# Kernel optimization log

Hardware: AMD Instinct MI355X
Metric: run time of the kernel (lower is better)

The kernel has to match this reference:

```python
import jax, jax.numpy as jnp
import numpy as np

TAU = 2.0  # LIF membrane time constant (spikingjelly default)
SCALE = 0.125

@jax.custom_vjp
def heaviside(x):
    return (x >= 0).astype(x.dtype)

def _hv_fwd(x):
    return heaviside(x), x

def _hv_bwd(x, g):
    s = jax.nn.sigmoid(4.0 * x)  # sigmoid surrogate, alpha=4
    return (g * 4.0 * s * (1.0 - s),)

heaviside.defvjp(_hv_fwd, _hv_bwd)

def lif(x, v_th):
    """Multi-step LIF over leading time axis. x: [T, ...]. decay_input, hard reset to 0."""
    def step(v, xt):
        v = v + (xt - v) / TAU
        s = heaviside(v - v_th)
        return v * (1.0 - s), s
    return jax.lax.scan(step, jnp.zeros_like(x[0]), x)[1]

def conv1x1(x, w, b=None):
    # x: [T,B,C,N], w: [O,C]
    y = jnp.einsum('oc,tbcn->tbon', w, x)
    if b is not None:
        y = y + b[None, None, :, None]
    return y

def bn(x, p, eps=1e-5):
    # inference-mode BatchNorm1d over channel axis; p: [4,C] = gamma,beta,mean,var
    g, b, m, v = p[0], p[1], p[2], p[3]
    inv = g / jnp.sqrt(v + eps)
    return x * inv[None, None, :, None] + (b - m * inv)[None, None, :, None]

def setup_inputs() -> dict:
    key = jax.random.key(0)
    ks = jax.random.split(key, 10)
    T, B, C, H, W = 4, 32, 512, 16, 16
    wscale = 1.0 / np.sqrt(C)
    def bn_params(k):
        k1, k2, k3, k4 = jax.random.split(k, 4)
        gamma = 1.0 + 0.1 * jax.random.normal(k1, (C,))
        beta = 0.1 * jax.random.normal(k2, (C,))
        mean = 0.1 * jax.random.normal(k3, (C,))
        var = 1.0 + 0.1 * jax.random.uniform(k4, (C,))
        return jnp.stack([gamma, beta, mean, var])
    return {
        'x': jax.random.normal(ks[0], (T, B, C, H, W), dtype=jnp.float32),
        'res_attn': jnp.zeros((1,), dtype=jnp.float32),
        'q_w': wscale * jax.random.normal(ks[1], (C, C), dtype=jnp.float32),
        'k_w': wscale * jax.random.normal(ks[2], (C, C), dtype=jnp.float32),
        'v_w': wscale * jax.random.normal(ks[3], (C, C), dtype=jnp.float32),
        'proj_w': wscale * jax.random.normal(ks[4], (C, C), dtype=jnp.float32),
        'proj_b': 0.01 * jax.random.normal(ks[5], (C,), dtype=jnp.float32),
        'q_bn': bn_params(ks[6]),
        'k_bn': bn_params(ks[7]),
        'v_bn': bn_params(ks[8]),
        'p_bn': bn_params(ks[9]),
    }

def reference(x, res_attn, q_w, k_w, v_w, proj_w, proj_b, q_bn, k_bn, v_bn, p_bn):
    T, B, C, H, W = x.shape
    num_heads = 8
    d = C // num_heads
    N = H * W
    xf = x.reshape(T, B, C, N)

    def branch(w, p, v_th):
        return lif(bn(conv1x1(xf, w), p), v_th)

    def to_heads(t):  # [T,B,C,N] -> [T,B,h,N,d]
        return t.transpose(0, 1, 3, 2).reshape(T, B, N, num_heads, d).transpose(0, 1, 3, 2, 4)

    q = to_heads(branch(q_w, q_bn, 1.0))
    k = to_heads(branch(k_w, k_bn, 1.0))
    v = to_heads(branch(v_w, v_bn, 1.0))

    # linear (non-softmax) attention: q @ (k^T @ v) * scale
    kv = jnp.einsum('tbhnd,tbhne->tbhde', k, v)
    a = jnp.einsum('tbhnd,tbhde->tbhne', q, kv) * SCALE  # [T,B,h,N,d]

    # [T,B,h,N,d] -> transpose(3,4) -> [T,B,h,d,N] -> [T,B,C,N]
    a = jnp.swapaxes(a, 3, 4).reshape(T, B, C, N)
    a = lif(a, 0.5)  # attn_lif with v_threshold=0.5

    out = conv1x1(a, proj_w, proj_b)
    out = bn(out, p_bn).reshape(T, B, C, H, W)
    out = lif(out, 1.0)
    return out, v
```

## Files before the change

### kernel.cpp

```cpp
#include <hip/hip_runtime.h>
#include <stdint.h>

#define T_ 4
#define B_ 32
#define C_ 512
#define N_ 256
#define NH_ 8
#define NB_ (N_ / 8)
#define BITS_BYTES_ ((size_t)(T_ * B_ * C_) * NB_)

typedef float f32x2 __attribute__((ext_vector_type(2)));

__device__ __forceinline__ f32x2 pk_mul_d(f32x2 a, f32x2 b) {
  f32x2 r;
  asm("v_pk_mul_f32 %0, %1, %2" : "=v"(r) : "v"(a), "v"(b));
  return r;
}
__device__ __forceinline__ f32x2 pk_mul_x(f32x2 a, f32x2 b) {
  f32x2 r;
  asm("v_pk_mul_f32 %0, %1, %2 op_sel:[0,1] op_sel_hi:[1,0]"
      : "=v"(r) : "v"(a), "v"(b));
  return r;
}
__device__ __forceinline__ void pk_add_acc(f32x2& acc, f32x2 p) {
  asm("v_pk_add_f32 %0, %0, %1" : "+v"(acc) : "v"(p));
}
__device__ __forceinline__ void pk_fma_d(f32x2& acc, f32x2 a, f32x2 b) {
  asm("v_pk_fma_f32 %0, %1, %2, %0" : "+v"(acc) : "v"(a), "v"(b));
}
__device__ __forceinline__ void pk_fma_x(f32x2& acc, f32x2 a, f32x2 b) {
  asm("v_pk_fma_f32 %0, %1, %2, %0 op_sel:[0,1,0] op_sel_hi:[1,0,1]"
      : "+v"(acc) : "v"(a), "v"(b));
}


__global__ __launch_bounds__(256, 2) void qkv_gemm_lif(
    const float* __restrict__ x, const float* __restrict__ wq,
    const float* __restrict__ wk, const float* __restrict__ wv,
    const float* __restrict__ bnq, const float* __restrict__ bnk,
    const float* __restrict__ bnv,
    uint8_t* __restrict__ sbits, float* __restrict__ out1) {
#pragma clang fp contract(off)
  const int br = blockIdx.z;
  const int b  = blockIdx.y;
  const int ot = blockIdx.x >> 1, nt = blockIdx.x & 1;
  const float* w = (br == 0) ? wq : (br == 1) ? wk : wv;
  const float* bn = (br == 0) ? bnq : (br == 1) ? bnk : bnv;
  uint8_t* sb = sbits + (size_t)br * BITS_BYTES_;

  const int tid = threadIdx.x;
  const int tx = tid & 15, ty = tid >> 4;
  const int o0 = ot * 64, n0 = nt * 128;

  __shared__ float As[16][64];
  __shared__ float Bs[16][128];

  float inv[4], add[4];
#pragma unroll
  for (int i = 0; i < 4; ++i) {
    int o = o0 + ty * 4 + i;
    float g = bn[o], be = bn[C_ + o], mm = bn[2 * C_ + o], va = bn[3 * C_ + o];
    float iv = g / sqrtf(va + 1e-5f);
    inv[i] = iv;
    add[i] = be - mm * iv;
  }

  float vst[4][8];
#pragma unroll
  for (int i = 0; i < 4; ++i)
#pragma unroll
    for (int j = 0; j < 8; ++j) vst[i][j] = 0.f;

  for (int t = 0; t < T_; ++t) {
    const float* xb = x + (size_t)(t * B_ + b) * (C_ * N_);
    f32x2 acc_d[2][4], acc_x[2][4];
#pragma unroll
    for (int ip = 0; ip < 2; ++ip)
#pragma unroll
      for (int jp = 0; jp < 4; ++jp) {
        acc_d[ip][jp] = (f32x2){0.f, 0.f};
        acc_x[ip][jp] = (f32x2){0.f, 0.f};
      }

    for (int kc = 0; kc < C_; kc += 16) {
      int o = tid & 63, kq = (tid >> 6) * 4;
      float4 a4 = *(const float4*)(w + (size_t)(o0 + o) * C_ + kc + kq);
      int fr = tid >> 5, fq = (tid & 31) * 4;
      int fr2 = (tid + 256) >> 5, fq2 = ((tid + 256) & 31) * 4;
      float4 b40 = *(const float4*)(xb + (size_t)(kc + fr) * N_ + n0 + fq);
      float4 b41 = *(const float4*)(xb + (size_t)(kc + fr2) * N_ + n0 + fq2);
      __syncthreads();
      As[kq + 0][o] = a4.x; As[kq + 1][o] = a4.y;
      As[kq + 2][o] = a4.z; As[kq + 3][o] = a4.w;
      *(float4*)(&Bs[fr][fq]) = b40;
      *(float4*)(&Bs[fr2][fq2]) = b41;
      __syncthreads();
#pragma unroll
      for (int k = 0; k < 16; ++k) {
        float4 av4 = *(const float4*)(&As[k][ty * 4]);
        float4 bq0 = *(const float4*)(&Bs[k][tx * 4]);
        float4 bq1 = *(const float4*)(&Bs[k][64 + tx * 4]);
        f32x2 a2[2] = {(f32x2){av4.x, av4.y}, (f32x2){av4.z, av4.w}};
        f32x2 b2[4] = {(f32x2){bq0.x, bq0.y}, (f32x2){bq0.z, bq0.w},
                       (f32x2){bq1.x, bq1.y}, (f32x2){bq1.z, bq1.w}};
#pragma unroll
        for (int ip = 0; ip < 2; ++ip)
#pragma unroll
          for (int jp = 0; jp < 4; ++jp) {
            f32x2 pd = pk_mul_d(a2[ip], b2[jp]);
            f32x2 px = pk_mul_x(a2[ip], b2[jp]);
            pk_add_acc(acc_d[ip][jp], pd);
            pk_add_acc(acc_x[ip][jp], px);
          }
      }
    }
    __syncthreads();

    {
      size_t tb = (size_t)(t * B_ + b);
      unsigned nibsA = 0, nibsB = 0;
#pragma unroll
      for (int i = 0; i < 4; ++i) {
#pragma unroll
        for (int jj = 0; jj < 8; ++jj) {
          int ip = i >> 1, il = i & 1, jp = jj >> 1, jl = jj & 1;
          float a = (il == jl) ? acc_d[ip][jp][il] : acc_x[ip][jp][il];
          float y0 = a * inv[i];
          float y = y0 + add[i];
          float d = y - vst[i][jj];
          float vs = vst[i][jj] + d * 0.5f;
          unsigned sp = (vs >= 1.0f) ? 1u : 0u;
          vst[i][jj] = sp ? 0.f : vs;
          if (jj < 4) nibsA |= sp << (4 * i + jj);
          else        nibsB |= sp << (4 * i + jj - 4);
        }
      }
      unsigned oA = __shfl_xor(nibsA, 1);
      unsigned oB = __shfl_xor(nibsB, 1);
      int m = tx >> 1;
      if ((tx & 1) == 0) {
#pragma unroll
        for (int i = 0; i < 4; ++i) {
          int o = o0 + ty * 4 + i;
          unsigned byte_ = ((nibsA >> (4 * i)) & 0xF) | (((oA >> (4 * i)) & 0xF) << 4);
          sb[(tb * C_ + o) * NB_ + (n0 >> 3) + m] = (uint8_t)byte_;
        }
      } else {
#pragma unroll
        for (int i = 0; i < 4; ++i) {
          int o = o0 + ty * 4 + i;
          unsigned byte_ = ((oB >> (4 * i)) & 0xF) | (((nibsB >> (4 * i)) & 0xF) << 4);
          sb[(tb * C_ + o) * NB_ + (n0 >> 3) + 8 + m] = (uint8_t)byte_;
        }
      }
      if (br == 2) {
#pragma unroll
        for (int i = 0; i < 4; ++i) {
          int o = o0 + ty * 4 + i;
          int h = o >> 6, dd = o & 63;
          size_t base = ((tb * NH_ + h) * (size_t)N_) * 64 + dd;
#pragma unroll
          for (int jj = 0; jj < 8; ++jj) {
            int n = n0 + ((jj < 4) ? (tx * 4 + jj) : (64 + tx * 4 + jj - 4));
            unsigned sp = (jj < 4) ? ((nibsA >> (4 * i + jj)) & 1u)
                                   : ((nibsB >> (4 * i + jj - 4)) & 1u);
            out1[base + (size_t)n * 64] = sp ? 1.0f : 0.0f;
          }
        }
      }
    }
  }
}

__global__ __launch_bounds__(512, 1) void attn_lif(
    const uint8_t* __restrict__ bits, uint8_t* __restrict__ abits) {
#pragma clang fp contract(off)
  const unsigned long long* qb = (const unsigned long long*)bits;
  const unsigned long long* kb = qb + BITS_BYTES_ / 8;
  const unsigned long long* vb = kb + BITS_BYTES_ / 8;
  unsigned long long* ap = (unsigned long long*)abits;

  const int h = blockIdx.x, b = blockIdx.y;
  const int tid = threadIdx.x;
  const int lane = tid & 63, wave = tid >> 6;
  const int nw = wave & 3, eh = wave >> 2;

  __shared__ unsigned long long kbl[64][4];
  __shared__ unsigned long long vbl[64][4];
  __shared__ float kvl[64][64];

  float state[32];
#pragma unroll
  for (int e = 0; e < 32; ++e) state[e] = 0.f;

  for (int t = 0; t < T_; ++t) {
    size_t row0 = (size_t)(t * B_ + b) * C_ + h * 64;
    {
      int i = tid & 255, c = i >> 2, w = i & 3;
      if (tid < 256) kbl[c][w] = kb[(row0 + c) * 4 + w];
      else           vbl[c][w] = vb[(row0 + c) * 4 + w];
    }
    __syncthreads();
    {
      int d = tid & 63, eb = (tid >> 6) * 8;
#pragma unroll
      for (int e2 = 0; e2 < 8; ++e2) {
        int e = eb + e2;
        int s = 0;
#pragma unroll
        for (int w = 0; w < 4; ++w) s += __popcll(kbl[d][w] & vbl[e][w]);
        kvl[d][e] = (float)s;
      }
    }
    __syncthreads();
    float acc[32];
#pragma unroll
    for (int e = 0; e < 32; ++e) acc[e] = 0.f;
    for (int d = 0; d < 64; ++d) {
      unsigned long long qw = qb[(row0 + d) * 4 + nw];
      float qf = (float)(unsigned)((qw >> lane) & 1ULL);
      const float* kr = &kvl[d][eh * 32];
#pragma unroll
      for (int e = 0; e < 32; ++e) acc[e] = acc[e] + qf * kr[e];
    }
    {
#pragma unroll
      for (int e2 = 0; e2 < 32; ++e2) {
        int e = eh * 32 + e2;
        float a = acc[e2] * 0.125f;
        float d0 = a - state[e2];
        float vs = state[e2] + d0 * 0.5f;
        int sp = (vs >= 0.5f) ? 1 : 0;
        state[e2] = sp ? 0.f : vs;
        unsigned long long m = __ballot(sp);
        if (lane == 0) ap[(row0 + e) * 4 + nw] = m;
      }
    }
    __syncthreads();
  }
}

__global__ __launch_bounds__(256, 2) void proj_gemm_lif(
    const uint8_t* __restrict__ ab, const float* __restrict__ wp,
    const float* __restrict__ pb, const float* __restrict__ bnp,
    float* __restrict__ out0) {
  const int b = blockIdx.y;
  const int ot = blockIdx.x >> 1, nt = blockIdx.x & 1;
  const int tid = threadIdx.x;
  const int tx = tid & 15, ty = tid >> 4;
  const int o0 = ot * 64, n0 = nt * 128;

  __shared__ float As[16][64];
  __shared__ float Bs[16][128];

  float inv[4], add[4], bias[4];
  {
#pragma clang fp contract(off)
#pragma unroll
    for (int i = 0; i < 4; ++i) {
      int o = o0 + ty * 4 + i;
      float g = bnp[o], be = bnp[C_ + o], mm = bnp[2 * C_ + o], va = bnp[3 * C_ + o];
      float iv = g / sqrtf(va + 1e-5f);
      inv[i] = iv;
      add[i] = be - mm * iv;
      bias[i] = pb[o];
    }
  }

  float vst[4][8];
#pragma unroll
  for (int i = 0; i < 4; ++i)
#pragma unroll
    for (int j = 0; j < 8; ++j) vst[i][j] = 0.f;

  for (int t = 0; t < T_; ++t) {
    f32x2 acc_d[2][4], acc_x[2][4];
#pragma unroll
    for (int ip = 0; ip < 2; ++ip)
#pragma unroll
      for (int jp = 0; jp < 4; ++jp) {
        acc_d[ip][jp] = (f32x2){0.f, 0.f};
        acc_x[ip][jp] = (f32x2){0.f, 0.f};
      }
    size_t tb = (size_t)(t * B_ + b);

    for (int kc = 0; kc < C_; kc += 16) {
      {
        int o = tid & 63, kq = (tid >> 6) * 4;
        float4 a4 = *(const float4*)(wp + (size_t)(o0 + o) * C_ + kc + kq);
        As[kq + 0][o] = a4.x; As[kq + 1][o] = a4.y;
        As[kq + 2][o] = a4.z; As[kq + 3][o] = a4.w;
      }
      {
        int r = tid >> 4, q16 = tid & 15;
        uint8_t by = ab[(tb * C_ + kc + r) * NB_ + (n0 >> 3) + q16];
        int nb = q16 * 8;
#pragma unroll
        for (int j = 0; j < 8; ++j) Bs[r][nb + j] = (float)((by >> j) & 1);
      }
      __syncthreads();
#pragma unroll
      for (int k = 0; k < 16; ++k) {
        float4 av4 = *(const float4*)(&As[k][ty * 4]);
        float4 bq0 = *(const float4*)(&Bs[k][tx * 4]);
        float4 bq1 = *(const float4*)(&Bs[k][64 + tx * 4]);
        f32x2 a2[2] = {(f32x2){av4.x, av4.y}, (f32x2){av4.z, av4.w}};
        f32x2 b2[4] = {(f32x2){bq0.x, bq0.y}, (f32x2){bq0.z, bq0.w},
                       (f32x2){bq1.x, bq1.y}, (f32x2){bq1.z, bq1.w}};
#pragma unroll
        for (int ip = 0; ip < 2; ++ip)
#pragma unroll
          for (int jp = 0; jp < 4; ++jp) {
            pk_fma_d(acc_d[ip][jp], a2[ip], b2[jp]);
            pk_fma_x(acc_x[ip][jp], a2[ip], b2[jp]);
          }
      }
      __syncthreads();
    }

    {
#pragma clang fp contract(off)
#pragma unroll
      for (int i = 0; i < 4; ++i) {
        int o = o0 + ty * 4 + i;
        float4 r0, r1;
#pragma unroll
        for (int jj = 0; jj < 8; ++jj) {
          int ip = i >> 1, il = i & 1, jp = jj >> 1, jl = jj & 1;
          float a = (il == jl) ? acc_d[ip][jp][il] : acc_x[ip][jp][il];
          float y1 = a + bias[i];
          float y2 = y1 * inv[i];
          float y = y2 + add[i];
          float d0 = y - vst[i][jj];
          float vs = vst[i][jj] + d0 * 0.5f;
          int sp = (vs >= 1.0f) ? 1 : 0;
          vst[i][jj] = sp ? 0.f : vs;
          if (jj < 4) (&r0.x)[jj] = sp ? 1.0f : 0.0f;
          else        (&r1.x)[jj - 4] = sp ? 1.0f : 0.0f;
        }
        float* dst = out0 + (tb * C_ + o) * N_ + n0;
        *(float4*)(dst + tx * 4) = r0;
        *(float4*)(dst + 64 + tx * 4) = r1;
      }
    }
  }
}


extern "C" void kernel_launch(void* const* d_in, const int* in_sizes, int n_in,
                              void* d_out, int out_size, void* d_ws, size_t ws_size,
                              hipStream_t stream) {
  const float* x   = (const float*)d_in[0];
  const float* qw  = (const float*)d_in[2];
  const float* kw  = (const float*)d_in[3];
  const float* vw  = (const float*)d_in[4];
  const float* pw  = (const float*)d_in[5];
  const float* pbb = (const float*)d_in[6];
  const float* qbn = (const float*)d_in[7];
  const float* kbn = (const float*)d_in[8];
  const float* vbn = (const float*)d_in[9];
  const float* pbn = (const float*)d_in[10];

  uint8_t* bits  = (uint8_t*)d_ws;
  uint8_t* abits = bits + 3 * BITS_BYTES_;

  float* out0 = (float*)d_out;
  float* out1 = out0 + (size_t)T_ * B_ * C_ * N_;

  qkv_gemm_lif<<<dim3(16, 32, 3), dim3(256), 0, stream>>>(
      x, qw, kw, vw, qbn, kbn, vbn, bits, out1);
  attn_lif<<<dim3(8, 32), dim3(512), 0, stream>>>(bits, abits);
  proj_gemm_lif<<<dim3(16, 32), dim3(256), 0, stream>>>(abits, pw, pbb, pbn,
                                                        out0);
}
```

Before: 1.304 ms.

## Double-buffer shared-memory tiles in QKV and projection GEMM kernels

Both GEMM+LIF kernels now use two shared-memory buffers for the A and B tiles. The loads for the next K-chunk are issued from global memory before computing on the current chunk, then stored into the other buffer. This removes one barrier per iteration and hides global load latency behind the FMA loop. In exchange it doubles LDS use per block and adds register pressure from the prefetched values, which may hurt occupancy.

```diff
diff --git a/kernel.cpp b/kernel.cpp
--- a/kernel.cpp
+++ b/kernel.cpp
@@ -52,8 +52,8 @@
   const int tx = tid & 15, ty = tid >> 4;
   const int o0 = ot * 64, n0 = nt * 128;
 
-  __shared__ float As[16][64];
-  __shared__ float Bs[16][128];
+  __shared__ float As[2][16][64];
+  __shared__ float Bs[2][16][128];
 
   float inv[4], add[4];
 #pragma unroll
@@ -71,6 +71,10 @@
 #pragma unroll
     for (int j = 0; j < 8; ++j) vst[i][j] = 0.f;
 
+  const int sa_o = tid & 63, sa_kq = (tid >> 6) * 4;
+  const int fr = tid >> 5, fq = (tid & 31) * 4;
+  const int fr2 = (tid + 256) >> 5, fq2 = ((tid + 256) & 31) * 4;
+
   for (int t = 0; t < T_; ++t) {
     const float* xb = x + (size_t)(t * B_ + b) * (C_ * N_);
     f32x2 acc_d[2][4], acc_x[2][4];
@@ -82,24 +86,32 @@
         acc_x[ip][jp] = (f32x2){0.f, 0.f};
       }
 
-    for (int kc = 0; kc < C_; kc += 16) {
-      int o = tid & 63, kq = (tid >> 6) * 4;
-      float4 a4 = *(const float4*)(w + (size_t)(o0 + o) * C_ + kc + kq);
-      int fr = tid >> 5, fq = (tid & 31) * 4;
-      int fr2 = (tid + 256) >> 5, fq2 = ((tid + 256) & 31) * 4;
-      float4 b40 = *(const float4*)(xb + (size_t)(kc + fr) * N_ + n0 + fq);
-      float4 b41 = *(const float4*)(xb + (size_t)(kc + fr2) * N_ + n0 + fq2);
+    {
+      float4 a4 = *(const float4*)(w + (size_t)(o0 + sa_o) * C_ + 0 + sa_kq);
+      float4 b40 = *(const float4*)(xb + (size_t)(0 + fr) * N_ + n0 + fq);
+      float4 b41 = *(const float4*)(xb + (size_t)(0 + fr2) * N_ + n0 + fq2);
       __syncthreads();
-      As[kq + 0][o] = a4.x; As[kq + 1][o] = a4.y;
-      As[kq + 2][o] = a4.z; As[kq + 3][o] = a4.w;
-      *(float4*)(&Bs[fr][fq]) = b40;
-      *(float4*)(&Bs[fr2][fq2]) = b41;
+      As[0][sa_kq + 0][sa_o] = a4.x; As[0][sa_kq + 1][sa_o] = a4.y;
+      As[0][sa_kq + 2][sa_o] = a4.z; As[0][sa_kq + 3][sa_o] = a4.w;
+      *(float4*)(&Bs[0][fr][fq]) = b40;
+      *(float4*)(&Bs[0][fr2][fq2]) = b41;
       __syncthreads();
+    }
+
+    for (int it = 0; it < 32; ++it) {
+      const int cur = it & 1;
+      float4 a4, b40, b41;
+      if (it < 31) {
+        int kc = (it + 1) * 16;
+        a4  = *(const float4*)(w + (size_t)(o0 + sa_o) * C_ + kc + sa_kq);
+        b40 = *(const float4*)(xb + (size_t)(kc + fr) * N_ + n0 + fq);
+        b41 = *(const float4*)(xb + (size_t)(kc + fr2) * N_ + n0 + fq2);
+      }
 #pragma unroll
       for (int k = 0; k < 16; ++k) {
-        float4 av4 = *(const float4*)(&As[k][ty * 4]);
-        float4 bq0 = *(const float4*)(&Bs[k][tx * 4]);
-        float4 bq1 = *(const float4*)(&Bs[k][64 + tx * 4]);
+        float4 av4 = *(const float4*)(&As[cur][k][ty * 4]);
+        float4 bq0 = *(const float4*)(&Bs[cur][k][tx * 4]);
+        float4 bq1 = *(const float4*)(&Bs[cur][k][64 + tx * 4]);
         f32x2 a2[2] = {(f32x2){av4.x, av4.y}, (f32x2){av4.z, av4.w}};
         f32x2 b2[4] = {(f32x2){bq0.x, bq0.y}, (f32x2){bq0.z, bq0.w},
                        (f32x2){bq1.x, bq1.y}, (f32x2){bq1.z, bq1.w}};
@@ -113,8 +125,15 @@
             pk_add_acc(acc_x[ip][jp], px);
           }
       }
-    }
-    __syncthreads();
+      if (it < 31) {
+        const int nxt = cur ^ 1;
+        As[nxt][sa_kq + 0][sa_o] = a4.x; As[nxt][sa_kq + 1][sa_o] = a4.y;
+        As[nxt][sa_kq + 2][sa_o] = a4.z; As[nxt][sa_kq + 3][sa_o] = a4.w;
+        *(float4*)(&Bs[nxt][fr][fq]) = b40;
+        *(float4*)(&Bs[nxt][fr2][fq2]) = b41;
+        __syncthreads();
+      }
+    }
 
     {
       size_t tb = (size_t)(t * B_ + b);
@@ -250,8 +269,8 @@
   const int tx = tid & 15, ty = tid >> 4;
   const int o0 = ot * 64, n0 = nt * 128;
 
-  __shared__ float As[16][64];
-  __shared__ float Bs[16][128];
+  __shared__ float As[2][16][64];
+  __shared__ float Bs[2][16][128];
 
   float inv[4], add[4], bias[4];
   {
@@ -273,6 +292,9 @@
 #pragma unroll
     for (int j = 0; j < 8; ++j) vst[i][j] = 0.f;
 
+  const int sa_o = tid & 63, sa_kq = (tid >> 6) * 4;
+  const int br_ = tid >> 4, bq16 = tid & 15;
+
   for (int t = 0; t < T_; ++t) {
     f32x2 acc_d[2][4], acc_x[2][4];
 #pragma unroll
@@ -284,26 +306,31 @@
       }
     size_t tb = (size_t)(t * B_ + b);
 
-    for (int kc = 0; kc < C_; kc += 16) {
-      {
-        int o = tid & 63, kq = (tid >> 6) * 4;
-        float4 a4 = *(const float4*)(wp + (size_t)(o0 + o) * C_ + kc + kq);
-        As[kq + 0][o] = a4.x; As[kq + 1][o] = a4.y;
-        As[kq + 2][o] = a4.z; As[kq + 3][o] = a4.w;
-      }
-      {
-        int r = tid >> 4, q16 = tid & 15;
-        uint8_t by = ab[(tb * C_ + kc + r) * NB_ + (n0 >> 3) + q16];
-        int nb = q16 * 8;
-#pragma unroll
-        for (int j = 0; j < 8; ++j) Bs[r][nb + j] = (float)((by >> j) & 1);
-      }
+    {
+      float4 a4 = *(const float4*)(wp + (size_t)(o0 + sa_o) * C_ + 0 + sa_kq);
+      uint8_t by = ab[(tb * C_ + 0 + br_) * NB_ + (n0 >> 3) + bq16];
       __syncthreads();
+      As[0][sa_kq + 0][sa_o] = a4.x; As[0][sa_kq + 1][sa_o] = a4.y;
+      As[0][sa_kq + 2][sa_o] = a4.z; As[0][sa_kq + 3][sa_o] = a4.w;
+      int nb = bq16 * 8;
+#pragma unroll
+      for (int j = 0; j < 8; ++j) Bs[0][br_][nb + j] = (float)((by >> j) & 1);
+      __syncthreads();
+    }
+
+    for (int it = 0; it < 32; ++it) {
+      const int cur = it & 1;
+      float4 a4; uint8_t by = 0;
+      if (it < 31) {
+        int kc = (it + 1) * 16;
+        a4 = *(const float4*)(wp + (size_t)(o0 + sa_o) * C_ + kc + sa_kq);
+        by = ab[(tb * C_ + kc + br_) * NB_ + (n0 >> 3) + bq16];
+      }
 #pragma unroll
       for (int k = 0; k < 16; ++k) {
-        float4 av4 = *(const float4*)(&As[k][ty * 4]);
-        float4 bq0 = *(const float4*)(&Bs[k][tx * 4]);
-        float4 bq1 = *(const float4*)(&Bs[k][64 + tx * 4]);
+        float4 av4 = *(const float4*)(&As[cur][k][ty * 4]);
+        float4 bq0 = *(const float4*)(&Bs[cur][k][tx * 4]);
+        float4 bq1 = *(const float4*)(&Bs[cur][k][64 + tx * 4]);
         f32x2 a2[2] = {(f32x2){av4.x, av4.y}, (f32x2){av4.z, av4.w}};
         f32x2 b2[4] = {(f32x2){bq0.x, bq0.y}, (f32x2){bq0.z, bq0.w},
                        (f32x2){bq1.x, bq1.y}, (f32x2){bq1.z, bq1.w}};
@@ -315,7 +342,15 @@
             pk_fma_x(acc_x[ip][jp], a2[ip], b2[jp]);
           }
       }
-      __syncthreads();
+      if (it < 31) {
+        const int nxt = cur ^ 1;
+        As[nxt][sa_kq + 0][sa_o] = a4.x; As[nxt][sa_kq + 1][sa_o] = a4.y;
+        As[nxt][sa_kq + 2][sa_o] = a4.z; As[nxt][sa_kq + 3][sa_o] = a4.w;
+        int nb = bq16 * 8;
+#pragma unroll
+        for (int j = 0; j < 8; ++j) Bs[nxt][br_][nb + j] = (float)((by >> j) & 1);
+        __syncthreads();
+      }
     }
 
     {
```

Result: faster. 1.275 ms (-2.2%).
